# Optimization experiments

Hardware: AMD Instinct MI355X
Metric: run time of the kernel (lower is better)

The kernel has to match this reference:

```python
import jax, jax.numpy as jnp
import numpy as np

B, N, C, NUM_HEADS, POOL = 8, 3136, 768, 12, 3
HIDDEN = 4 * C
EPS = 1e-5


def setup_inputs() -> dict:
    key = jax.random.key(0)
    ks = jax.random.split(key, 6)
    g = lambda k, shape, sc: (jax.random.normal(k, shape, jnp.float32) * sc)
    return {
        "x": g(ks[0], (B, N, C), 1.0),
        "ln1_g": jnp.ones((C,), jnp.float32),
        "ln1_b": jnp.zeros((C,), jnp.float32),
        "qkv_w": g(ks[1], (3 * C, C), 0.02),
        "proj_w": g(ks[2], (C, C), 0.02),
        "proj_b": jnp.zeros((C,), jnp.float32),
        "ln2_g": jnp.ones((C,), jnp.float32),
        "ln2_b": jnp.zeros((C,), jnp.float32),
        "fc1_w": g(ks[3], (HIDDEN, C), 0.02),
        "fc1_b": jnp.zeros((HIDDEN,), jnp.float32),
        "fc2_w": g(ks[4], (C, HIDDEN), 0.02),
        "fc2_b": jnp.zeros((C,), jnp.float32),
    }


def _ln(z, g, b):
    m = jnp.mean(z, axis=-1, keepdims=True)
    v = jnp.var(z, axis=-1, keepdims=True)
    return (z - m) * jax.lax.rsqrt(v + EPS) * g + b


def _avgpool_seq(t):
    # t: (B, H, N, hd); AvgPool1d(kernel=3, stride=3, pad=1, count_include_pad=True)
    s = jax.lax.reduce_window(
        t, jnp.float32(0), jax.lax.add,
        window_dimensions=(1, 1, POOL, 1),
        window_strides=(1, 1, POOL, 1),
        padding=((0, 0), (0, 0), (POOL // 2, POOL // 2), (0, 0)),
    )
    return s / POOL


def reference(x, ln1_g, ln1_b, qkv_w, proj_w, proj_b, ln2_g, ln2_b, fc1_w, fc1_b, fc2_w, fc2_b):
    b, n, c = x.shape
    hd = c // NUM_HEADS
    # --- attention sublayer ---
    h = _ln(x, ln1_g, ln1_b)
    qkv = (h @ qkv_w.T).reshape(b, n, 3, NUM_HEADS, hd).transpose(2, 0, 3, 1, 4)
    q, k, v = qkv[0], qkv[1], qkv[2]  # each (B, H, N, hd)
    k = _avgpool_seq(k)  # (B, H, Np, hd)
    v = _avgpool_seq(v)
    attn = jnp.einsum('bhqd,bhkd->bhqk', q, k) * (hd ** -0.5)
    attn = jax.nn.softmax(attn, axis=-1)
    o = jnp.einsum('bhqk,bhkd->bhqd', attn, v)
    o = o.transpose(0, 2, 1, 3).reshape(b, n, c)
    x = x + (o @ proj_w.T + proj_b)
    # --- MLP sublayer ---
    h2 = _ln(x, ln2_g, ln2_b)
    m = jax.nn.gelu(h2 @ fc1_w.T + fc1_b, approximate=False)
    m = m @ fc2_w.T + fc2_b
    return x + m
```

## Files before the change

kernel.cpp:

```cpp
#include <hip/hip_runtime.h>
#include <hip/hip_bf16.h>
#include <math.h>

#define B_   8
#define N_   3136
#define C_   768
#define H_   12
#define HD_  64
#define NP_  1046
#define NPP_ 1056
#define M_   (B_*N_)

typedef __bf16 bf16x8 __attribute__((ext_vector_type(8)));
typedef float  f32x4  __attribute__((ext_vector_type(4)));

__device__ __forceinline__ float bf2f(__hip_bfloat16 v){ return __bfloat162float(v); }
__device__ __forceinline__ __hip_bfloat16 f2bf(float v){ return __float2bfloat16(v); }

__device__ __forceinline__ void load_lds16(const void* g, void* l) {
  __builtin_amdgcn_global_load_lds(
      (const __attribute__((address_space(1))) unsigned int*)g,
      (__attribute__((address_space(3))) unsigned int*)l, 16, 0, 0);
}

#define MFMA16(a,b,c) __builtin_amdgcn_mfma_f32_16x16x32_bf16((a),(b),(c),0,0,0)

__device__ __forceinline__ float gelu_f(float v) {
  float y = 1.5957691f * (v + 0.044715f * v * v * v);
  float e = __expf(y);
  return v * e / (e + 1.0f);
}

__global__ void cvt_kernel(const float* __restrict__ s0, __hip_bfloat16* __restrict__ d0, int n0,
                           const float* __restrict__ s1, __hip_bfloat16* __restrict__ d1, int n1,
                           const float* __restrict__ s2, __hip_bfloat16* __restrict__ d2, int n2,
                           const float* __restrict__ s3, __hip_bfloat16* __restrict__ d3, int n3) {
  int i = blockIdx.x * 256 + threadIdx.x;
  if (i < n0) d0[i] = f2bf(s0[i]);
  i -= n0;
  if (i >= 0 && i < n1) d1[i] = f2bf(s1[i]);
  i -= n1;
  if (i >= 0 && i < n2) d2[i] = f2bf(s2[i]);
  i -= n2;
  if (i >= 0 && i < n3) d3[i] = f2bf(s3[i]);
}

__global__ __launch_bounds__(256)
void ln_kernel(const float* __restrict__ x, const float* __restrict__ g,
               const float* __restrict__ bta, __hip_bfloat16* __restrict__ out) {
  const size_t row = blockIdx.x;
  const float* xr = x + row * C_;
  const int t = threadIdx.x;
  float v0 = xr[t], v1 = xr[t + 256], v2 = xr[t + 512];
  float s  = v0 + v1 + v2;
  float s2 = v0*v0 + v1*v1 + v2*v2;
  #pragma unroll
  for (int off = 32; off > 0; off >>= 1) { s += __shfl_down(s, off); s2 += __shfl_down(s2, off); }
  __shared__ float ws1[4], ws2[4];
  if ((t & 63) == 0) { ws1[t >> 6] = s; ws2[t >> 6] = s2; }
  __syncthreads();
  float S  = ws1[0] + ws1[1] + ws1[2] + ws1[3];
  float S2 = ws2[0] + ws2[1] + ws2[2] + ws2[3];
  float mean = S * (1.0f / C_);
  float var  = S2 * (1.0f / C_) - mean * mean;
  float rstd = rsqrtf(var + 1e-5f);
  __hip_bfloat16* orow = out + row * C_;
  orow[t]       = f2bf((v0 - mean) * rstd * g[t]       + bta[t]);
  orow[t + 256] = f2bf((v1 - mean) * rstd * g[t + 256] + bta[t + 256]);
  orow[t + 512] = f2bf((v2 - mean) * rstd * g[t + 512] + bta[t + 512]);
}

__global__ void pool_kernel(const __hip_bfloat16* __restrict__ qkv,
                            __hip_bfloat16* __restrict__ kp,
                            __hip_bfloat16* __restrict__ vpt) {
  int idx = blockIdx.x * 256 + threadIdx.x;
  int d  = idx & 63;
  int np = (idx >> 6) % NPP_;
  int bh = idx / (NPP_ * 64);
  int b = bh / H_, h = bh % H_;
  float ak = 0.f, av = 0.f;
  if (np < NP_) {
    #pragma unroll
    for (int t = 0; t < 3; ++t) {
      int n = np * 3 - 1 + t;
      if (n >= 0 && n < N_) {
        size_t base = ((size_t)b * N_ + n) * (3 * C_) + h * HD_ + d;
        ak += bf2f(qkv[base + C_]);
        av += bf2f(qkv[base + 2 * C_]);
      }
    }
    ak *= (1.0f / 3.0f); av *= (1.0f / 3.0f);
  }
  int c = np & 31;
  int lhi = c >> 3, rr = c & 7;
  int p = (rr < 4) ? (lhi * 4 + rr) : (16 + lhi * 4 + rr - 4);
  kp[((size_t)bh * NPP_ + (np - c) + p) * HD_ + d] = f2bf(ak);
  vpt[((size_t)bh * HD_ + d) * NPP_ + np] = f2bf(av);
}

__global__ __launch_bounds__(256)
void attn_kernel(const __hip_bfloat16* __restrict__ qkv,
                 const __hip_bfloat16* __restrict__ kp,
                 const __hip_bfloat16* __restrict__ vpt,
                 __hip_bfloat16* __restrict__ o) {
  __shared__ __align__(16) char smem[16384];
  const int tid  = threadIdx.x;
  const int lane = tid & 63;
  const int w    = tid >> 6;
  const int bh = blockIdx.y;
  const int b = bh / H_, h = bh % H_;
  const int q0 = blockIdx.x * 128 + w * 32;
  const int l15 = lane & 15, lhi = lane >> 4;

  bf16x8 qf[2][2];
  #pragma unroll
  for (int f = 0; f < 2; ++f) {
    int qrow = q0 + f * 16 + l15;
    if (qrow >= N_) qrow = N_ - 1;
    const __hip_bfloat16* qptr = qkv + ((size_t)(b * N_ + qrow)) * (3 * C_) + h * HD_ + lhi * 8;
    qf[f][0] = *(const bf16x8*)(qptr);
    qf[f][1] = *(const bf16x8*)(qptr + 32);
    #pragma unroll
    for (int i = 0; i < 8; ++i) {
      qf[f][0][i] = qf[f][0][i] * (__bf16)0.125f;
      qf[f][1][i] = qf[f][1][i] * (__bf16)0.125f;
    }
  }

  const char* kp_base  = (const char*)(kp  + (size_t)bh * NPP_ * HD_);
  const char* vpt_base = (const char*)(vpt + (size_t)bh * HD_ * NPP_);
  const int krow_s = tid >> 3;
  const int pK = (tid & 7) * 16;
  const int srcKoff = krow_s * 128 + (pK ^ ((krow_s & 7) << 4));
  const int qV = pK ^ ((krow_s & 7) << 4);
  const int vrow_s = 2 * krow_s + (qV >> 6);
  const int srcVoff = vrow_s * (NPP_ * 2) + (qV & 63);

  char* dstK[2] = { smem + 0    + w * 1024, smem + 8192 + 0    + w * 1024 };
  char* dstV[2] = { smem + 4096 + w * 1024, smem + 8192 + 4096 + w * 1024 };

  load_lds16(kp_base + srcKoff, dstK[0]);
  load_lds16(vpt_base + srcVoff, dstV[0]);
  __syncthreads();

  f32x4 oacc[2][4] = {};
  float lp[2] = {0.f, 0.f};

  for (int kc = 0; kc < NPP_; kc += 32) {
    const int cur = (kc >> 5) & 1;
    if (kc + 32 < NPP_) {
      load_lds16(kp_base + (size_t)(kc + 32) * 128 + srcKoff, dstK[cur ^ 1]);
      load_lds16(vpt_base + (size_t)(kc + 32) * 2 + srcVoff, dstV[cur ^ 1]);
    }
    const char* sK = smem + cur * 8192;
    const char* sV = smem + cur * 8192 + 4096;

    bf16x8 ka0 = *(const bf16x8*)(sK + l15 * 128        + (( 0 + 16 * lhi) ^ ((l15 & 7) << 4)));
    bf16x8 ka1 = *(const bf16x8*)(sK + l15 * 128        + ((64 + 16 * lhi) ^ ((l15 & 7) << 4)));
    bf16x8 kb0 = *(const bf16x8*)(sK + (16 + l15) * 128 + (( 0 + 16 * lhi) ^ ((l15 & 7) << 4)));
    bf16x8 kb1 = *(const bf16x8*)(sK + (16 + l15) * 128 + ((64 + 16 * lhi) ^ ((l15 & 7) << 4)));
    bf16x8 vf[4];
    #pragma unroll
    for (int nb = 0; nb < 4; ++nb) {
      int row = nb * 16 + l15;
      int Lv = row >> 1;
      int p = (((row & 1) * 64) + 16 * lhi) ^ ((Lv & 7) << 4);
      vf[nb] = *(const bf16x8*)(sV + Lv * 128 + p);
    }

    #pragma unroll
    for (int f = 0; f < 2; ++f) {
      f32x4 s0 = {}, s1 = {};
      s0 = MFMA16(ka0, qf[f][0], s0);
      s0 = MFMA16(ka1, qf[f][1], s0);
      s1 = MFMA16(kb0, qf[f][0], s1);
      s1 = MFMA16(kb1, qf[f][1], s1);
      bf16x8 pa;
      #pragma unroll
      for (int r = 0; r < 4; ++r) {
        float p0 = (kc + lhi * 8 + r     < NP_) ? __expf(s0[r]) : 0.f;
        float p1 = (kc + lhi * 8 + 4 + r < NP_) ? __expf(s1[r]) : 0.f;
        lp[f] += p0 + p1;
        pa[r]     = (__bf16)p0;
        pa[r + 4] = (__bf16)p1;
      }
      #pragma unroll
      for (int nb = 0; nb < 4; ++nb)
        oacc[f][nb] = MFMA16(pa, vf[nb], oacc[f][nb]);
    }
    __syncthreads();
  }

  #pragma unroll
  for (int f = 0; f < 2; ++f) {
    float lpf = lp[f];
    lpf += __shfl_xor(lpf, 16);
    lpf += __shfl_xor(lpf, 32);
    #pragma unroll
    for (int r = 0; r < 4; ++r) {
      int orow = q0 + f * 16 + lhi * 4 + r;
      if (orow < N_) {
        float inv = 1.0f / __shfl(lpf, lhi * 4 + r);
        size_t rowbase = ((size_t)(b * N_ + orow)) * C_ + h * HD_;
        #pragma unroll
        for (int nb = 0; nb < 4; ++nb)
          o[rowbase + nb * 16 + l15] = f2bf(oacc[f][nb][r] * inv);
      }
    }
  }
}

__global__ __launch_bounds__(256, 2)
void gemm128(const __hip_bfloat16* __restrict__ A,
             const __hip_bfloat16* __restrict__ Bt,
             const float* __restrict__ bias,
             const float* __restrict__ res, float* __restrict__ out,
             int M, int N, int K) {
  __shared__ __align__(16) __hip_bfloat16 sA[4][128 * 32];
  __shared__ __align__(16) __hip_bfloat16 sB[4][128 * 32];
  const int tid = threadIdx.x, lane = tid & 63, wid = tid >> 6;
  const int wr = wid >> 1, wc = wid & 1;
  const int l15 = lane & 15, lhi = lane >> 4;

  const int nwg = gridDim.x;
  const int ntx = N >> 7;
  const int qq = nwg >> 3, rr8 = nwg & 7;
  const int xcd = blockIdx.x & 7, off8 = blockIdx.x >> 3;
  const int wg = (xcd < rr8 ? xcd * (qq + 1) : rr8 * (qq + 1) + (xcd - rr8) * qq) + off8;
  const long row0 = (long)(wg / ntx) * 128;
  const long col0 = (long)(wg % ntx) * 128;

  const size_t ldb = (size_t)K * 2;
  const int R = tid >> 2;
  const int scol = ((tid & 3) * 16) ^ ((R & 3) << 4);
  const char* gA = (const char*)A  + (size_t)(row0 + R) * ldb + scol;
  const char* gB = (const char*)Bt + (size_t)(col0 + R) * ldb + scol;

  const int fsw = (lhi * 16) ^ ((l15 & 3) << 4);

  f32x4 acc[4][4] = {};

#define STG(b, t) { \
    const char* ga_ = gA + (size_t)(t) * 64; \
    const char* gb_ = gB + (size_t)(t) * 64; \
    char* la_ = (char*)&sA[b][0] + wid * 1024; \
    char* lb_ = (char*)&sB[b][0] + wid * 1024; \
    load_lds16(ga_, la_); \
    load_lds16(ga_ + 64 * ldb, la_ + 4096); \
    load_lds16(gb_, lb_); \
    load_lds16(gb_ + 64 * ldb, lb_ + 4096); }

  const int NT = K >> 5;
  STG(0, 0); STG(1, 1); STG(2, 2);
  asm volatile("s_waitcnt vmcnt(8)" ::: "memory");
  __syncthreads();

  for (int t = 0; t < NT; ++t) {
    const int b = t & 3;
    bf16x8 af[4], bfv[4];
    const char* pa_ = (const char*)&sA[b][0] + (wr * 64 + l15) * 64 + fsw;
    const char* pb_ = (const char*)&sB[b][0] + (wc * 64 + l15) * 64 + fsw;
    #pragma unroll
    for (int m = 0; m < 4; ++m) af[m]  = *(const bf16x8*)(pa_ + m * 16 * 64);
    #pragma unroll
    for (int n = 0; n < 4; ++n) bfv[n] = *(const bf16x8*)(pb_ + n * 16 * 64);
    if (t + 3 < NT) {
      STG((t + 3) & 3, t + 3);
      asm volatile("s_waitcnt vmcnt(8)" ::: "memory");
    } else if (t + 2 < NT) {
      asm volatile("s_waitcnt vmcnt(4)" ::: "memory");
    } else if (t + 1 < NT) {
      asm volatile("s_waitcnt vmcnt(0)" ::: "memory");
    }
    __builtin_amdgcn_sched_barrier(0);
    __builtin_amdgcn_s_barrier();
    __builtin_amdgcn_sched_barrier(0);
    __builtin_amdgcn_s_setprio(1);
    #pragma unroll
    for (int m = 0; m < 4; ++m)
      #pragma unroll
      for (int n = 0; n < 4; ++n)
        acc[m][n] = MFMA16(af[m], bfv[n], acc[m][n]);
    __builtin_amdgcn_s_setprio(0);
  }
#undef STG

  #pragma unroll
  for (int m = 0; m < 4; ++m) {
    long rbase = row0 + wr * 64 + m * 16 + lhi * 4;
    #pragma unroll
    for (int n = 0; n < 4; ++n) {
      long col = col0 + wc * 64 + n * 16 + l15;
      #pragma unroll
      for (int r = 0; r < 4; ++r) {
        size_t idx = (size_t)(rbase + r) * N + col;
        out[idx] = acc[m][n][r] + bias[col] + res[idx];
      }
    }
  }
}

template<int EPI>
__global__ __launch_bounds__(512, 2)
void gemm256(const __hip_bfloat16* __restrict__ A,
             const __hip_bfloat16* __restrict__ Bt,
             const float* __restrict__ bias,
             const float* res, void* outv,
             int M, int N, int K) {
  extern __shared__ __align__(16) char lds[];
  const int tid = threadIdx.x;
  const int lane = tid & 63;
  const int wid = tid >> 6;
  const int wr = wid >> 2;
  const int wc = wid & 3;
  const int l15 = lane & 15, lhi = lane >> 4;

  const int nwg = gridDim.x;
  const int ntx = N >> 8;
  const int qq = nwg >> 3, rr8 = nwg & 7;
  const int xcd = blockIdx.x & 7, off8 = blockIdx.x >> 3;
  const int wg = (xcd < rr8 ? xcd * (qq + 1) : rr8 * (qq + 1) + (xcd - rr8) * qq) + off8;
  const long row0 = (long)(wg / ntx) * 256;
  const long col0 = (long)(wg % ntx) * 256;

  const size_t ldb = (size_t)K * 2;
  const int srow = wid * 16 + (lane >> 2);
  const int scol = ((lane & 3) * 16) ^ (lane & 32);
  const char* gA = (const char*)A  + (size_t)(row0 + srow) * ldb + scol;
  const char* gB = (const char*)Bt + (size_t)(col0 + srow) * ldb + scol;

#define STAGEH(op, t, kh, bb) { \
    const char* g_ = (op ? gB : gA) + (size_t)(t) * 128 + (kh) * 64; \
    char* l_ = lds + ((op) ? 65536 : 0) + (bb) * 32768 + (kh) * 16384 + wid * 1024; \
    load_lds16(g_, l_); \
    load_lds16(g_ + 128 * ldb, l_ + 8192); \
  }

  const int fragswz = (lhi * 16) ^ ((l15 & 8) << 2);
  const char* ldsA = lds + wr * 8192 + l15 * 64 + fragswz;
  const char* ldsB = lds + 65536 + wc * 4096 + l15 * 64 + fragswz;

  f32x4 acc[8][4] = {};
  bf16x8 bfr[4];

#define VM4 asm volatile("s_waitcnt vmcnt(4)" ::: "memory")
#define SBAR() { __builtin_amdgcn_sched_barrier(0); __builtin_amdgcn_s_barrier(); __builtin_amdgcn_sched_barrier(0); }

#define PHASE(bb, ks, mq, STG, VM) { \
    const char* pA_ = ldsA + (bb) * 32768 + (ks) * 16384 + (mq) * 4096; \
    bf16x8 afr[4]; \
    _Pragma("unroll") for (int i_ = 0; i_ < 4; ++i_) afr[i_] = *(const bf16x8*)(pA_ + i_ * 1024); \
    if ((mq) == 0) { \
      const char* pB_ = ldsB + (bb) * 32768 + (ks) * 16384; \
      _Pragma("unroll") for (int j_ = 0; j_ < 4; ++j_) bfr[j_] = *(const bf16x8*)(pB_ + j_ * 1024); \
    } \
    STG; \
    VM; \
    SBAR(); \
    __builtin_amdgcn_s_setprio(1); \
    _Pragma("unroll") for (int i_ = 0; i_ < 4; ++i_) \
      _Pragma("unroll") for (int j_ = 0; j_ < 4; ++j_) \
        acc[(mq) * 4 + i_][j_] = MFMA16(afr[i_], bfr[j_], acc[(mq) * 4 + i_][j_]); \
    __builtin_amdgcn_s_setprio(0); \
    SBAR(); \
  }

  STAGEH(0, 0, 0, 0); STAGEH(1, 0, 0, 0);
  STAGEH(0, 0, 1, 0); STAGEH(1, 0, 1, 0);
  STAGEH(0, 1, 0, 1); STAGEH(1, 1, 0, 1);
  VM4;
  SBAR();

  const int NT = K >> 6;
  for (int it = 0; it < (NT >> 1); ++it) {
    const int u = 2 * it;
    const bool s2 = (u + 2) < NT, s3 = (u + 3) < NT;
    PHASE(0, 0, 0, STAGEH(0, u + 1, 1, 1), );
    PHASE(0, 0, 1, STAGEH(1, u + 1, 1, 1), );
    PHASE(0, 1, 0, if (s2) STAGEH(0, u + 2, 0, 0), );
    PHASE(0, 1, 1, if (s2) STAGEH(1, u + 2, 0, 0), VM4);
    PHASE(1, 0, 0, if (s2) STAGEH(0, u + 2, 1, 0), );
    PHASE(1, 0, 1, if (s2) STAGEH(1, u + 2, 1, 0), );
    PHASE(1, 1, 0, if (s3) STAGEH(0, u + 3, 0, 1), );
    PHASE(1, 1, 1, if (s3) STAGEH(1, u + 3, 0, 1), VM4);
  }
#undef PHASE
#undef STAGEH
#undef VM4
#undef SBAR

  #pragma unroll
  for (int mf = 0; mf < 8; ++mf) {
    long rbase = row0 + wr * 128 + mf * 16 + lhi * 4;
    #pragma unroll
    for (int nf = 0; nf < 4; ++nf) {
      long col = col0 + wc * 64 + nf * 16 + l15;
      #pragma unroll
      for (int r = 0; r < 4; ++r) {
        size_t idx = (size_t)(rbase + r) * N + col;
        float v = acc[mf][nf][r];
        if (EPI == 0) {
          ((__hip_bfloat16*)outv)[idx] = f2bf(v);
        } else if (EPI == 1) {
          ((float*)outv)[idx] = v + bias[col] + res[idx];
        } else {
          ((__hip_bfloat16*)outv)[idx] = f2bf(gelu_f(v + bias[col]));
        }
      }
    }
  }
}

extern "C" void kernel_launch(void* const* d_in, const int* in_sizes, int n_in,
                              void* d_out, int out_size, void* d_ws, size_t ws_size,
                              hipStream_t stream) {
  const float* x      = (const float*)d_in[0];
  const float* ln1_g  = (const float*)d_in[1];
  const float* ln1_b  = (const float*)d_in[2];
  const float* qkv_w  = (const float*)d_in[3];
  const float* proj_w = (const float*)d_in[4];
  const float* proj_b = (const float*)d_in[5];
  const float* ln2_g  = (const float*)d_in[6];
  const float* ln2_b  = (const float*)d_in[7];
  const float* fc1_w  = (const float*)d_in[8];
  const float* fc1_b  = (const float*)d_in[9];
  const float* fc2_w  = (const float*)d_in[10];
  const float* fc2_b  = (const float*)d_in[11];
  float* out = (float*)d_out;

  char* ws = (char*)d_ws;
  __hip_bfloat16* wqkv  = (__hip_bfloat16*)(ws + 0);
  __hip_bfloat16* wproj = (__hip_bfloat16*)(ws + 3538944);
  __hip_bfloat16* wfc1  = (__hip_bfloat16*)(ws + 4718592);
  __hip_bfloat16* wfc2  = (__hip_bfloat16*)(ws + 9437184);
  __hip_bfloat16* hbuf  = (__hip_bfloat16*)(ws + 14155776);
  __hip_bfloat16* obuf  = (__hip_bfloat16*)(ws + 52690944);
  __hip_bfloat16* kpb   = (__hip_bfloat16*)(ws + 91226112);
  __hip_bfloat16* vptb  = (__hip_bfloat16*)(ws + 104202240);
  __hip_bfloat16* big   = (__hip_bfloat16*)(ws + 117178368);
  const size_t WS_NEEDED = 117178368ull + 154140672ull;
  if (ws_size < WS_NEEDED) return;

  hipFuncSetAttribute((const void*)gemm256<0>, hipFuncAttributeMaxDynamicSharedMemorySize, 131072);
  hipFuncSetAttribute((const void*)gemm256<2>, hipFuncAttributeMaxDynamicSharedMemorySize, 131072);

  {
    int n0 = 2304 * 768, n1 = 768 * 768, n2 = 3072 * 768, n3 = 768 * 3072;
    int tot = n0 + n1 + n2 + n3;
    cvt_kernel<<<(tot + 255) / 256, 256, 0, stream>>>(qkv_w, wqkv, n0, proj_w, wproj, n1,
                                                      fc1_w, wfc1, n2, fc2_w, wfc2, n3);
  }

  ln_kernel<<<M_, 256, 0, stream>>>(x, ln1_g, ln1_b, hbuf);
  gemm256<0><<<(M_ / 256) * (2304 / 256), 512, 131072, stream>>>(hbuf, wqkv, nullptr, nullptr, big, M_, 2304, 768);
  pool_kernel<<<(96 * NPP_ * 64) / 256, 256, 0, stream>>>(big, kpb, vptb);
  attn_kernel<<<dim3((N_ + 127) / 128, B_ * H_), 256, 0, stream>>>(big, kpb, vptb, obuf);
  gemm128<<<(M_ / 128) * (768 / 128), 256, 0, stream>>>(obuf, wproj, proj_b, x, out, M_, 768, 768);

  ln_kernel<<<M_, 256, 0, stream>>>(out, ln2_g, ln2_b, hbuf);
  gemm256<2><<<(M_ / 256) * (3072 / 256), 512, 131072, stream>>>(hbuf, wfc1, fc1_b, nullptr, big, M_, 3072, 768);
  gemm128<<<(M_ / 128) * (768 / 128), 256, 0, stream>>>(big, wfc2, fc2_b, out, out, M_, 768, 3072);
}
```

Measured before the change: 746.2 us.

## Pool LN output before K/V projection to shrink K/V GEMM

Result: faster. 700.5 us (-6.1%).

```diff
diff --git a/kernel.cpp b/kernel.cpp
--- a/kernel.cpp
+++ b/kernel.cpp
@@ -10,6 +10,7 @@
 #define NP_  1046
 #define NPP_ 1056
 #define M_   (B_*N_)
+#define MKV_ (B_*NPP_)
 
 typedef __bf16 bf16x8 __attribute__((ext_vector_type(8)));
 typedef float  f32x4  __attribute__((ext_vector_type(4)));
@@ -70,36 +71,52 @@
   orow[t + 512] = f2bf((v2 - mean) * rstd * g[t + 512] + bta[t + 512]);
 }
 
-__global__ void pool_kernel(const __hip_bfloat16* __restrict__ qkv,
-                            __hip_bfloat16* __restrict__ kp,
-                            __hip_bfloat16* __restrict__ vpt) {
+__global__ void pool_h_kernel(const __hip_bfloat16* __restrict__ h, __hip_bfloat16* __restrict__ hp) {
   int idx = blockIdx.x * 256 + threadIdx.x;
-  int d  = idx & 63;
-  int np = (idx >> 6) % NPP_;
-  int bh = idx / (NPP_ * 64);
-  int b = bh / H_, h = bh % H_;
-  float ak = 0.f, av = 0.f;
+  int c  = idx % C_;
+  int np = (idx / C_) % NPP_;
+  int b  = idx / (C_ * NPP_);
+  float a = 0.f;
   if (np < NP_) {
     #pragma unroll
     for (int t = 0; t < 3; ++t) {
       int n = np * 3 - 1 + t;
-      if (n >= 0 && n < N_) {
-        size_t base = ((size_t)b * N_ + n) * (3 * C_) + h * HD_ + d;
-        ak += bf2f(qkv[base + C_]);
-        av += bf2f(qkv[base + 2 * C_]);
-      }
-    }
-    ak *= (1.0f / 3.0f); av *= (1.0f / 3.0f);
-  }
-  int c = np & 31;
-  int lhi = c >> 3, rr = c & 7;
-  int p = (rr < 4) ? (lhi * 4 + rr) : (16 + lhi * 4 + rr - 4);
-  kp[((size_t)bh * NPP_ + (np - c) + p) * HD_ + d] = f2bf(ak);
-  vpt[((size_t)bh * HD_ + d) * NPP_ + np] = f2bf(av);
+      if (n >= 0 && n < N_) a += bf2f(h[((size_t)b * N_ + n) * C_ + c]);
+    }
+    a *= (1.0f / 3.0f);
+  }
+  hp[idx] = f2bf(a);
 }
 
 __global__ __launch_bounds__(256)
-void attn_kernel(const __hip_bfloat16* __restrict__ qkv,
+void rearr_kernel(const __hip_bfloat16* __restrict__ kv,
+                  __hip_bfloat16* __restrict__ kp, __hip_bfloat16* __restrict__ vpt) {
+  __shared__ __align__(16) __hip_bfloat16 sk[32][64], sv[32][64];
+  const int bh = blockIdx.y;
+  const int b = bh / H_, h = bh % H_;
+  const int np0 = blockIdx.x * 32;
+  const int t = threadIdx.x;
+  const int nl = t >> 3, d8 = (t & 7) * 8;
+  const __hip_bfloat16* src = kv + ((size_t)(b * NPP_) + np0 + nl) * 1536 + h * 64;
+  *(bf16x8*)&sk[nl][d8] = *(const bf16x8*)(src + d8);
+  *(bf16x8*)&sv[nl][d8] = *(const bf16x8*)(src + 768 + d8);
+  __syncthreads();
+  {
+    int lhi = nl >> 3, rr = nl & 7;
+    int p = (rr < 4) ? (lhi * 4 + rr) : (16 + lhi * 4 + rr - 4);
+    *(bf16x8*)(kp + ((size_t)bh * NPP_ + np0 + p) * 64 + d8) = *(const bf16x8*)&sk[nl][d8];
+  }
+  {
+    int d = t >> 2, n8 = (t & 3) * 8;
+    bf16x8 v;
+    #pragma unroll
+    for (int j = 0; j < 8; ++j) v[j] = sv[n8 + j][d];
+    *(bf16x8*)(vpt + ((size_t)bh * 64 + d) * NPP_ + np0 + n8) = v;
+  }
+}
+
+__global__ __launch_bounds__(256)
+void attn_kernel(const __hip_bfloat16* __restrict__ qb,
                  const __hip_bfloat16* __restrict__ kp,
                  const __hip_bfloat16* __restrict__ vpt,
                  __hip_bfloat16* __restrict__ o) {
@@ -117,7 +134,7 @@
   for (int f = 0; f < 2; ++f) {
     int qrow = q0 + f * 16 + l15;
     if (qrow >= N_) qrow = N_ - 1;
-    const __hip_bfloat16* qptr = qkv + ((size_t)(b * N_ + qrow)) * (3 * C_) + h * HD_ + lhi * 8;
+    const __hip_bfloat16* qptr = qb + ((size_t)(b * N_ + qrow)) * C_ + h * HD_ + lhi * 8;
     qf[f][0] = *(const bf16x8*)(qptr);
     qf[f][1] = *(const bf16x8*)(qptr + 32);
     #pragma unroll
@@ -295,6 +312,95 @@
       for (int r = 0; r < 4; ++r) {
         size_t idx = (size_t)(rbase + r) * N + col;
         out[idx] = acc[m][n][r] + bias[col] + res[idx];
+      }
+    }
+  }
+}
+
+__global__ __launch_bounds__(256, 2)
+void gemm128b(const __hip_bfloat16* __restrict__ A,
+              const __hip_bfloat16* __restrict__ Bt,
+              __hip_bfloat16* __restrict__ out,
+              int M, int N, int K) {
+  __shared__ __align__(16) __hip_bfloat16 sA[4][128 * 32];
+  __shared__ __align__(16) __hip_bfloat16 sB[4][128 * 32];
+  const int tid = threadIdx.x, lane = tid & 63, wid = tid >> 6;
+  const int wr = wid >> 1, wc = wid & 1;
+  const int l15 = lane & 15, lhi = lane >> 4;
+
+  const int nwg = gridDim.x;
+  const int ntx = N >> 7;
+  const int qq = nwg >> 3, rr8 = nwg & 7;
+  const int xcd = blockIdx.x & 7, off8 = blockIdx.x >> 3;
+  const int wg = (xcd < rr8 ? xcd * (qq + 1) : rr8 * (qq + 1) + (xcd - rr8) * qq) + off8;
+  const long row0 = (long)(wg / ntx) * 128;
+  const long col0 = (long)(wg % ntx) * 128;
+
+  const size_t ldb = (size_t)K * 2;
+  const int R = tid >> 2;
+  const int scol = ((tid & 3) * 16) ^ ((R & 3) << 4);
+  const char* gA = (const char*)A  + (size_t)(row0 + R) * ldb + scol;
+  const char* gB = (const char*)Bt + (size_t)(col0 + R) * ldb + scol;
+
+  const int fsw = (lhi * 16) ^ ((l15 & 3) << 4);
+
+  f32x4 acc[4][4] = {};
+
+#define STG(b, t) { \
+    const char* ga_ = gA + (size_t)(t) * 64; \
+    const char* gb_ = gB + (size_t)(t) * 64; \
+    char* la_ = (char*)&sA[b][0] + wid * 1024; \
+    char* lb_ = (char*)&sB[b][0] + wid * 1024; \
+    load_lds16(ga_, la_); \
+    load_lds16(ga_ + 64 * ldb, la_ + 4096); \
+    load_lds16(gb_, lb_); \
+    load_lds16(gb_ + 64 * ldb, lb_ + 4096); }
+
+  const int NT = K >> 5;
+  STG(0, 0); STG(1, 1); STG(2, 2);
+  asm volatile("s_waitcnt vmcnt(8)" ::: "memory");
+  __syncthreads();
+
+  for (int t = 0; t < NT; ++t) {
+    const int b = t & 3;
+    bf16x8 af[4], bfv[4];
+    const char* pa_ = (const char*)&sA[b][0] + (wr * 64 + l15) * 64 + fsw;
+    const char* pb_ = (const char*)&sB[b][0] + (wc * 64 + l15) * 64 + fsw;
+    #pragma unroll
+    for (int m = 0; m < 4; ++m) af[m]  = *(const bf16x8*)(pa_ + m * 16 * 64);
+    #pragma unroll
+    for (int n = 0; n < 4; ++n) bfv[n] = *(const bf16x8*)(pb_ + n * 16 * 64);
+    if (t + 3 < NT) {
+      STG((t + 3) & 3, t + 3);
+      asm volatile("s_waitcnt vmcnt(8)" ::: "memory");
+    } else if (t + 2 < NT) {
+      asm volatile("s_waitcnt vmcnt(4)" ::: "memory");
+    } else if (t + 1 < NT) {
+      asm volatile("s_waitcnt vmcnt(0)" ::: "memory");
+    }
+    __builtin_amdgcn_sched_barrier(0);
+    __builtin_amdgcn_s_barrier();
+    __builtin_amdgcn_sched_barrier(0);
+    __builtin_amdgcn_s_setprio(1);
+    #pragma unroll
+    for (int m = 0; m < 4; ++m)
+      #pragma unroll
+      for (int n = 0; n < 4; ++n)
+        acc[m][n] = MFMA16(af[m], bfv[n], acc[m][n]);
+    __builtin_amdgcn_s_setprio(0);
+  }
+#undef STG
+
+  #pragma unroll
+  for (int m = 0; m < 4; ++m) {
+    long rbase = row0 + wr * 64 + m * 16 + lhi * 4;
+    #pragma unroll
+    for (int n = 0; n < 4; ++n) {
+      long col = col0 + wc * 64 + n * 16 + l15;
+      #pragma unroll
+      for (int r = 0; r < 4; ++r) {
+        size_t idx = (size_t)(rbase + r) * N + col;
+        out[idx] = f2bf(acc[m][n][r]);
       }
     }
   }
@@ -441,7 +547,10 @@
   const size_t WS_NEEDED = 117178368ull + 154140672ull;
   if (ws_size < WS_NEEDED) return;
 
-  hipFuncSetAttribute((const void*)gemm256<0>, hipFuncAttributeMaxDynamicSharedMemorySize, 131072);
+  __hip_bfloat16* qb   = big;
+  __hip_bfloat16* kvb  = (__hip_bfloat16*)((char*)big + 38535168);
+  __hip_bfloat16* hp   = (__hip_bfloat16*)((char*)big + 64487424);
+
   hipFuncSetAttribute((const void*)gemm256<2>, hipFuncAttributeMaxDynamicSharedMemorySize, 131072);
 
   {
@@ -452,9 +561,11 @@
   }
 
   ln_kernel<<<M_, 256, 0, stream>>>(x, ln1_g, ln1_b, hbuf);
-  gemm256<0><<<(M_ / 256) * (2304 / 256), 512, 131072, stream>>>(hbuf, wqkv, nullptr, nullptr, big, M_, 2304, 768);
-  pool_kernel<<<(96 * NPP_ * 64) / 256, 256, 0, stream>>>(big, kpb, vptb);
-  attn_kernel<<<dim3((N_ + 127) / 128, B_ * H_), 256, 0, stream>>>(big, kpb, vptb, obuf);
+  gemm128b<<<(M_ / 128) * (768 / 128), 256, 0, stream>>>(hbuf, wqkv, qb, M_, 768, 768);
+  pool_h_kernel<<<(B_ * NPP_ * C_) / 256, 256, 0, stream>>>(hbuf, hp);
+  gemm128b<<<(MKV_ / 128) * (1536 / 128), 256, 0, stream>>>(hp, wqkv + 768 * 768, kvb, MKV_, 1536, 768);
+  rearr_kernel<<<dim3(NPP_ / 32, B_ * H_), 256, 0, stream>>>(kvb, kpb, vptb);
+  attn_kernel<<<dim3((N_ + 127) / 128, B_ * H_), 256, 0, stream>>>(qb, kpb, vptb, obuf);
   gemm128<<<(M_ / 128) * (768 / 128), 256, 0, stream>>>(obuf, wproj, proj_b, x, out, M_, 768, 768);
 
   ln_kernel<<<M_, 256, 0, stream>>>(out, ln2_g, ln2_b, hbuf);
```
